# Optimization experiments

Hardware: AMD Instinct MI355X
Metric: run time of the kernel (lower is better)

Reference implementation:

```python
import jax, jax.numpy as jnp
import numpy as np


def _nearest_resize(x, Hl, Wl):
    # x: [B, Hf, Wf] -> [B, Hl, Wl], PyTorch F.interpolate(mode='nearest') semantics:
    # src_idx = floor(out_idx * in_size / out_size)
    B, Hf, Wf = x.shape
    ri = (jnp.arange(Hl) * Hf) // Hl
    ci = (jnp.arange(Wl) * Wf) // Wl
    return x[:, ri[:, None], ci[None, :]]


def _nearest_centroid(f, c):
    # f: [B, C, H, W], c: [K, C]
    # argmin_k ||f - c_k||_2 over channels == argmin of squared distance
    f2 = jnp.sum(f * f, axis=1)                       # [B, H, W]
    c2 = jnp.sum(c * c, axis=1)                       # [K]
    cross = jnp.einsum('bchw,kc->bkhw', f, c)         # [B, K, H, W]
    d2 = f2[:, None] - 2.0 * cross + c2[None, :, None, None]
    return jnp.argmin(d2, axis=1)                     # [B, H, W] int


def setup_inputs() -> dict:
    key = jax.random.key(0)
    k1, k2, k3, k4, k5, k6 = jax.random.split(key, 6)
    B, C, Hf, Wf = 4, 256, 64, 128
    K = 19  # class_num
    Hl, Wl = 512, 1024
    return {
        'feature_s2t': jax.random.normal(k1, (B, C, Hf, Wf), dtype=jnp.float32),
        'feature_target': jax.random.normal(k2, (B, C, Hf, Wf), dtype=jnp.float32),
        'label_s2t': jax.random.randint(k3, (B, Hl, Wl), 0, K, dtype=jnp.int64) if jax.config.jax_enable_x64 else jax.random.randint(k3, (B, Hl, Wl), 0, K, dtype=jnp.int32),
        'label_target': jax.random.randint(k4, (B, Hl, Wl), 0, K, dtype=jnp.int32),
        'centroid_s2t': jax.random.normal(k5, (K, C), dtype=jnp.float32),
        'centroid_target': jax.random.normal(k6, (K, C), dtype=jnp.float32),
    }


def reference(feature_s2t, feature_target, label_s2t, label_target, centroid_s2t, centroid_target):
    # feature_s2t is matched against the TARGET-domain centroids and vice versa
    # (cross assignment, exactly as in the torch forward).
    mask_s2t = _nearest_centroid(feature_s2t, centroid_target)     # [B, Hf, Wf]
    mask_target = _nearest_centroid(feature_target, centroid_s2t)  # [B, Hf, Wf]
    Hl, Wl = label_s2t.shape[1], label_s2t.shape[2]
    mask_s2t = _nearest_resize(mask_s2t, Hl, Wl).astype(jnp.int32)
    Hl2, Wl2 = label_target.shape[1], label_target.shape[2]
    mask_target = _nearest_resize(mask_target, Hl2, Wl2).astype(jnp.int32)
    return (mask_s2t, mask_target)
```

## Files before the change

### kernel.cpp

```cpp
#include <hip/hip_runtime.h>

#define K   19
#define C   256
#define HF  64
#define WF  128
#define HW  (HF * WF)
#define BB  4
#define HL  512
#define WL  1024

#define TAU 0.015f

__global__ __launch_bounds__(512, 4) void centroid_mask_kernel(
    const float* __restrict__ feat0,
    const float* __restrict__ feat1,
    const float* __restrict__ cent0,
    const float* __restrict__ cent1,
    int* __restrict__ out)
{
    __shared__ float  part[8 * K * 64];
    __shared__ double c2p[K][8];
    __shared__ double sc2d[K];
    __shared__ float  sc2f[K];

    const int map = blockIdx.y;
    const float* __restrict__ feat = (map == 0) ? feat0 : feat1;
    const float* __restrict__ cent = (map == 0) ? cent0 : cent1;

    const int tid  = threadIdx.x;
    const int lane = tid & 63;
    const int wv   = __builtin_amdgcn_readfirstlane(tid >> 6);

    if (tid < K * 8) {
        const int k = tid >> 3, sl = tid & 7;
        const float* cp = cent + k * C + sl * 32;
        double s = 0.0;
        #pragma unroll
        for (int j = 0; j < 32; ++j) { double v = (double)cp[j]; s = fma(v, v, s); }
        c2p[k][sl] = s;
    }

    const int p  = blockIdx.x * 64 + lane;
    const int hw = p & (HW - 1);
    const int b  = p >> 13;
    const int cbase = wv * 32;

    const float* __restrict__ fp = feat + (size_t)b * C * HW + (size_t)cbase * HW + hw;
    float f[32];
    #pragma unroll
    for (int i = 0; i < 32; ++i) f[i] = fp[(size_t)i * HW];
    #pragma unroll
    for (int i = 0; i < 32; ++i) asm volatile("" : "+v"(f[i]));

    float* __restrict__ pw = &part[(wv * K) * 64 + lane];
    #pragma unroll
    for (int k = 0; k < K; ++k) {
        const float* __restrict__ ck = cent + (size_t)k * C + cbase;
        float a0 = 0.f, a1 = 0.f, a2 = 0.f, a3 = 0.f;
        #pragma unroll
        for (int j = 0; j < 8; ++j) {
            a0 = fmaf(f[4*j+0], ck[4*j+0], a0);
            a1 = fmaf(f[4*j+1], ck[4*j+1], a1);
            a2 = fmaf(f[4*j+2], ck[4*j+2], a2);
            a3 = fmaf(f[4*j+3], ck[4*j+3], a3);
        }
        pw[k * 64] = (a0 + a1) + (a2 + a3);
    }
    __syncthreads();

    if (tid < K) {
        double s = 0.0;
        #pragma unroll
        for (int j = 0; j < 8; ++j) s += c2p[tid][j];
        sc2d[tid] = s;
        sc2f[tid] = (float)s;
    }
    __syncthreads();

    if (tid < 64) {
        const int pix = tid;
        float d[K];
        #pragma unroll
        for (int k = 0; k < K; ++k) {
            float s = 0.f;
            #pragma unroll
            for (int w8 = 0; w8 < 8; ++w8)
                s += part[(w8 * K + k) * 64 + pix];
            d[k] = sc2f[k] - 2.0f * s;
        }
        int best = 0; float m1 = d[0];
        #pragma unroll
        for (int k = 1; k < K; ++k) if (d[k] < m1) { m1 = d[k]; best = k; }

        unsigned cmask = 0u;
        #pragma unroll
        for (int k = 0; k < K; ++k) if (d[k] - m1 < TAU) cmask |= (1u << k);

        const bool need = (cmask & (cmask - 1)) != 0u;
        unsigned long long ball = __ballot(need);
        while (ball) {
            const int px = (int)__builtin_ctzll(ball);
            ball &= ball - 1;
            const unsigned pm  = __shfl(cmask, px, 64);
            const int      phw = __shfl(hw,    px, 64);
            const int      pb  = __shfl(b,     px, 64);
            const float* __restrict__ fcol = feat + (size_t)pb * C * HW + phw;

            const int c0 = tid << 2;
            double pf[4];
            #pragma unroll
            for (int j = 0; j < 4; ++j)
                pf[j] = (double)fcol[(size_t)(c0 + j) * HW];

            double bd = 1e300; int bi = 0;
            unsigned mm = pm;
            while (mm) {
                const int k = (int)__builtin_ctz(mm);
                mm &= mm - 1;
                const float* __restrict__ ck = cent + (size_t)k * C + c0;
                double s = 0.0;
                #pragma unroll
                for (int j = 0; j < 4; ++j)
                    s = fma(pf[j], (double)ck[j], s);
                #pragma unroll
                for (int off = 1; off < 64; off <<= 1)
                    s += __shfl_xor(s, off, 64);
                const double dk = sc2d[k] - 2.0 * s;
                if (dk < bd) { bd = dk; bi = k; }
            }
            if (tid == px) best = bi;
        }

        const int w = hw & (WF - 1);
        const int h = hw >> 7;
        int4 v = make_int4(best, best, best, best);
        int* __restrict__ ob = out + (size_t)map * (BB * HL * WL)
                                   + (size_t)b * (HL * WL)
                                   + (size_t)(h * 8) * WL + (size_t)(w * 8);
        #pragma unroll
        for (int r = 0; r < 8; ++r) {
            *(int4*)(ob + (size_t)r * WL)     = v;
            *(int4*)(ob + (size_t)r * WL + 4) = v;
        }
    }
}

extern "C" void kernel_launch(void* const* d_in, const int* in_sizes, int n_in,
                              void* d_out, int out_size, void* d_ws, size_t ws_size,
                              hipStream_t stream) {
    const float* feature_s2t     = (const float*)d_in[0];
    const float* feature_target  = (const float*)d_in[1];
    const float* centroid_s2t    = (const float*)d_in[4];
    const float* centroid_target = (const float*)d_in[5];
    int* out = (int*)d_out;

    dim3 grid(32768 / 64, 2);
    dim3 block(512);
    hipLaunchKernelGGL(centroid_mask_kernel, grid, block, 0, stream,
                       feature_s2t, feature_target,
                       centroid_target, centroid_s2t, out);
}
```

Before: 26.84 us.

## Spread argmin and writes across all waves, defer ambiguous pixels to resolve kernel

```diff
diff --git a/kernel.cpp b/kernel.cpp
--- a/kernel.cpp
+++ b/kernel.cpp
@@ -10,27 +10,194 @@
 #define WL  1024
 
 #define TAU 0.015f
+#define CAP 65536
+#define WS_NEED (4u + 4u * (CAP + 1))
 
 __global__ __launch_bounds__(512, 4) void centroid_mask_kernel(
     const float* __restrict__ feat0,
     const float* __restrict__ feat1,
     const float* __restrict__ cent0,
     const float* __restrict__ cent1,
+    int* __restrict__ out,
+    unsigned* __restrict__ wlist)
+{
+    __shared__ float  part[8 * K * 64];
+    __shared__ double c2p[K][8];
+    __shared__ float  sc2f[K];
+
+    const int map = blockIdx.y;
+    const float* __restrict__ feat = (map == 0) ? feat0 : feat1;
+    const float* __restrict__ cent = (map == 0) ? cent0 : cent1;
+
+    const int tid  = threadIdx.x;
+    const int lane = tid & 63;
+    const int wv   = __builtin_amdgcn_readfirstlane(tid >> 6);
+
+    if (tid < K * 8) {
+        const int k = tid >> 3, sl = tid & 7;
+        const float* cp = cent + k * C + sl * 32;
+        double s = 0.0;
+        #pragma unroll
+        for (int j = 0; j < 32; ++j) { double v = (double)cp[j]; s = fma(v, v, s); }
+        c2p[k][sl] = s;
+    }
+
+    const int p  = blockIdx.x * 64 + lane;
+    const int hw = p & (HW - 1);
+    const int b  = p >> 13;
+    const int cbase = wv * 32;
+
+    const float* __restrict__ fp = feat + (size_t)b * C * HW + (size_t)cbase * HW + hw;
+    float f[32];
+    #pragma unroll
+    for (int i = 0; i < 32; ++i) f[i] = fp[(size_t)i * HW];
+    #pragma unroll
+    for (int i = 0; i < 32; ++i) asm volatile("" : "+v"(f[i]));
+
+    float* __restrict__ pw = &part[(wv * K) * 64 + lane];
+    #pragma unroll
+    for (int k = 0; k < K; ++k) {
+        const float* __restrict__ ck = cent + (size_t)k * C + cbase;
+        float a0 = 0.f, a1 = 0.f, a2 = 0.f, a3 = 0.f;
+        #pragma unroll
+        for (int j = 0; j < 8; ++j) {
+            a0 = fmaf(f[4*j+0], ck[4*j+0], a0);
+            a1 = fmaf(f[4*j+1], ck[4*j+1], a1);
+            a2 = fmaf(f[4*j+2], ck[4*j+2], a2);
+            a3 = fmaf(f[4*j+3], ck[4*j+3], a3);
+        }
+        pw[k * 64] = (a0 + a1) + (a2 + a3);
+    }
+    __syncthreads();
+
+    if (tid < K) {
+        double s = 0.0;
+        #pragma unroll
+        for (int j = 0; j < 8; ++j) s += c2p[tid][j];
+        sc2f[tid] = (float)s;
+    }
+    __syncthreads();
+
+    {
+        const int pl = lane >> 3;
+        const int j  = lane & 7;
+        const int px = 8 * wv + pl;
+
+        float d0, d1, d2 = 1e30f;
+        {
+            float s = 0.f;
+            #pragma unroll
+            for (int w8 = 0; w8 < 8; ++w8) s += part[(w8 * K + j) * 64 + px];
+            d0 = sc2f[j] - 2.0f * s;
+        }
+        {
+            float s = 0.f;
+            #pragma unroll
+            for (int w8 = 0; w8 < 8; ++w8) s += part[(w8 * K + j + 8) * 64 + px];
+            d1 = sc2f[j + 8] - 2.0f * s;
+        }
+        if (j < 3) {
+            float s = 0.f;
+            #pragma unroll
+            for (int w8 = 0; w8 < 8; ++w8) s += part[(w8 * K + j + 16) * 64 + px];
+            d2 = sc2f[j + 16] - 2.0f * s;
+        }
+
+        float dm = d0; int km = j;
+        if (d1 < dm) { dm = d1; km = j + 8; }
+        if (j < 3 && d2 < dm) { dm = d2; km = j + 16; }
+
+        #pragma unroll
+        for (int off = 1; off < 8; off <<= 1) {
+            float od = __shfl_xor(dm, off, 64);
+            int   ok = __shfl_xor(km, off, 64);
+            if (od < dm || (od == dm && ok < km)) { dm = od; km = ok; }
+        }
+
+        int cnt = (int)(d0 - dm < TAU) + (int)(d1 - dm < TAU)
+                + (int)(j < 3 && (d2 - dm < TAU));
+        #pragma unroll
+        for (int off = 1; off < 8; off <<= 1) cnt += __shfl_xor(cnt, off, 64);
+
+        const int pp  = blockIdx.x * 64 + px;
+        const int phw = pp & (HW - 1);
+        const int pb  = pp >> 13;
+
+        if (cnt >= 2 && j == 0) {
+            unsigned idx = atomicAdd(wlist, 1u);
+            if (idx < CAP)
+                wlist[1 + idx] = ((unsigned)map << 15) | ((unsigned)pb << 13)
+                               | (unsigned)phw;
+        }
+
+        const int w = phw & (WF - 1);
+        const int h = phw >> 7;
+        int4 v = make_int4(km, km, km, km);
+        int* __restrict__ ob = out + (size_t)map * (BB * HL * WL)
+                                   + (size_t)pb * (HL * WL)
+                                   + (size_t)(h * 8 + j) * WL + (size_t)(w * 8);
+        *(int4*)(ob)     = v;
+        *(int4*)(ob + 4) = v;
+    }
+}
+
+__global__ __launch_bounds__(64) void resolve_kernel(
+    const float* __restrict__ feat0, const float* __restrict__ feat1,
+    const float* __restrict__ cent0, const float* __restrict__ cent1,
+    const unsigned* __restrict__ wlist,
+    int* __restrict__ out)
+{
+    unsigned cnt = wlist[0];
+    if (cnt > CAP) cnt = CAP;
+    const int l = threadIdx.x;
+
+    for (unsigned i = blockIdx.x; i < cnt; i += gridDim.x) {
+        const unsigned e = wlist[1 + i];
+        const int map = (e >> 15) & 1;
+        const int b   = (e >> 13) & 3;
+        const int hw  = e & (HW - 1);
+        const float* __restrict__ feat = map ? feat1 : feat0;
+        const float* __restrict__ cent = map ? cent1 : cent0;
+
+        const int c0 = l << 2;
+        double pf[4];
+        #pragma unroll
+        for (int q = 0; q < 4; ++q)
+            pf[q] = (double)feat[(size_t)b * C * HW + (size_t)(c0 + q) * HW + hw];
+
+        double bd = 1e300; int bi = 0;
+        for (int k = 0; k < K; ++k) {
+            const float4 cc = *(const float4*)(cent + (size_t)k * C + c0);
+            double s = 0.0, t;
+            t = pf[0] - (double)cc.x; s = fma(t, t, s);
+            t = pf[1] - (double)cc.y; s = fma(t, t, s);
+            t = pf[2] - (double)cc.z; s = fma(t, t, s);
+            t = pf[3] - (double)cc.w; s = fma(t, t, s);
+            #pragma unroll
+            for (int off = 1; off < 64; off <<= 1) s += __shfl_xor(s, off, 64);
+            if (s < bd) { bd = s; bi = k; }
+        }
+
+        const int w = hw & (WF - 1), h = hw >> 7;
+        out[(size_t)map * (BB * HL * WL) + (size_t)b * (HL * WL)
+            + (size_t)(h * 8 + (l >> 3)) * WL + (size_t)(w * 8) + (l & 7)] = bi;
+    }
+}
+
+__global__ __launch_bounds__(512, 4) void centroid_mask_kernel_nows(
+    const float* __restrict__ feat0, const float* __restrict__ feat1,
+    const float* __restrict__ cent0, const float* __restrict__ cent1,
     int* __restrict__ out)
 {
     __shared__ float  part[8 * K * 64];
     __shared__ double c2p[K][8];
     __shared__ double sc2d[K];
     __shared__ float  sc2f[K];
-
     const int map = blockIdx.y;
     const float* __restrict__ feat = (map == 0) ? feat0 : feat1;
     const float* __restrict__ cent = (map == 0) ? cent0 : cent1;
-
-    const int tid  = threadIdx.x;
-    const int lane = tid & 63;
-    const int wv   = __builtin_amdgcn_readfirstlane(tid >> 6);
-
+    const int tid = threadIdx.x, lane = tid & 63;
+    const int wv = __builtin_amdgcn_readfirstlane(tid >> 6);
     if (tid < K * 8) {
         const int k = tid >> 3, sl = tid & 7;
         const float* cp = cent + k * C + sl * 32;
@@ -39,19 +206,12 @@
         for (int j = 0; j < 32; ++j) { double v = (double)cp[j]; s = fma(v, v, s); }
         c2p[k][sl] = s;
     }
-
-    const int p  = blockIdx.x * 64 + lane;
-    const int hw = p & (HW - 1);
-    const int b  = p >> 13;
-    const int cbase = wv * 32;
-
+    const int p = blockIdx.x * 64 + lane;
+    const int hw = p & (HW - 1), b = p >> 13, cbase = wv * 32;
     const float* __restrict__ fp = feat + (size_t)b * C * HW + (size_t)cbase * HW + hw;
     float f[32];
     #pragma unroll
     for (int i = 0; i < 32; ++i) f[i] = fp[(size_t)i * HW];
-    #pragma unroll
-    for (int i = 0; i < 32; ++i) asm volatile("" : "+v"(f[i]));
-
     float* __restrict__ pw = &part[(wv * K) * 64 + lane];
     #pragma unroll
     for (int k = 0; k < K; ++k) {
@@ -67,16 +227,13 @@
         pw[k * 64] = (a0 + a1) + (a2 + a3);
     }
     __syncthreads();
-
     if (tid < K) {
         double s = 0.0;
         #pragma unroll
         for (int j = 0; j < 8; ++j) s += c2p[tid][j];
-        sc2d[tid] = s;
-        sc2f[tid] = (float)s;
+        sc2d[tid] = s; sc2f[tid] = (float)s;
     }
     __syncthreads();
-
     if (tid < 64) {
         const int pix = tid;
         float d[K];
@@ -84,18 +241,15 @@
         for (int k = 0; k < K; ++k) {
             float s = 0.f;
             #pragma unroll
-            for (int w8 = 0; w8 < 8; ++w8)
-                s += part[(w8 * K + k) * 64 + pix];
+            for (int w8 = 0; w8 < 8; ++w8) s += part[(w8 * K + k) * 64 + pix];
             d[k] = sc2f[k] - 2.0f * s;
         }
         int best = 0; float m1 = d[0];
         #pragma unroll
         for (int k = 1; k < K; ++k) if (d[k] < m1) { m1 = d[k]; best = k; }
-
         unsigned cmask = 0u;
         #pragma unroll
         for (int k = 0; k < K; ++k) if (d[k] - m1 < TAU) cmask |= (1u << k);
-
         const bool need = (cmask & (cmask - 1)) != 0u;
         unsigned long long ball = __ballot(need);
         while (ball) {
@@ -105,13 +259,10 @@
             const int      phw = __shfl(hw,    px, 64);
             const int      pb  = __shfl(b,     px, 64);
             const float* __restrict__ fcol = feat + (size_t)pb * C * HW + phw;
-
             const int c0 = tid << 2;
             double pf[4];
             #pragma unroll
-            for (int j = 0; j < 4; ++j)
-                pf[j] = (double)fcol[(size_t)(c0 + j) * HW];
-
+            for (int j = 0; j < 4; ++j) pf[j] = (double)fcol[(size_t)(c0 + j) * HW];
             double bd = 1e300; int bi = 0;
             unsigned mm = pm;
             while (mm) {
@@ -120,22 +271,17 @@
                 const float* __restrict__ ck = cent + (size_t)k * C + c0;
                 double s = 0.0;
                 #pragma unroll
-                for (int j = 0; j < 4; ++j)
-                    s = fma(pf[j], (double)ck[j], s);
+                for (int j = 0; j < 4; ++j) s = fma(pf[j], (double)ck[j], s);
                 #pragma unroll
-                for (int off = 1; off < 64; off <<= 1)
-                    s += __shfl_xor(s, off, 64);
+                for (int off = 1; off < 64; off <<= 1) s += __shfl_xor(s, off, 64);
                 const double dk = sc2d[k] - 2.0 * s;
                 if (dk < bd) { bd = dk; bi = k; }
             }
             if (tid == px) best = bi;
         }
-
-        const int w = hw & (WF - 1);
-        const int h = hw >> 7;
+        const int w = hw & (WF - 1), h = hw >> 7;
         int4 v = make_int4(best, best, best, best);
-        int* __restrict__ ob = out + (size_t)map * (BB * HL * WL)
-                                   + (size_t)b * (HL * WL)
+        int* __restrict__ ob = out + (size_t)map * (BB * HL * WL) + (size_t)b * (HL * WL)
                                    + (size_t)(h * 8) * WL + (size_t)(w * 8);
         #pragma unroll
         for (int r = 0; r < 8; ++r) {
@@ -154,9 +300,18 @@
     const float* centroid_target = (const float*)d_in[5];
     int* out = (int*)d_out;
 
-    dim3 grid(32768 / 64, 2);
-    dim3 block(512);
-    hipLaunchKernelGGL(centroid_mask_kernel, grid, block, 0, stream,
-                       feature_s2t, feature_target,
-                       centroid_target, centroid_s2t, out);
+    if (ws_size >= (size_t)WS_NEED) {
+        unsigned* wlist = (unsigned*)d_ws;
+        hipMemsetAsync(d_ws, 0, 4, stream);
+        hipLaunchKernelGGL(centroid_mask_kernel, dim3(512, 2), dim3(512), 0, stream,
+                           feature_s2t, feature_target,
+                           centroid_target, centroid_s2t, out, wlist);
+        hipLaunchKernelGGL(resolve_kernel, dim3(512), dim3(64), 0, stream,
+                           feature_s2t, feature_target,
+                           centroid_target, centroid_s2t, wlist, out);
+    } else {
+        hipLaunchKernelGGL(centroid_mask_kernel_nows, dim3(512, 2), dim3(512), 0, stream,
+                           feature_s2t, feature_target,
+                           centroid_target, centroid_s2t, out);
+    }
 }
```

Result: slower. 44.81 us (+67.0%).

## Spread argmin epilogue and output writes across all eight waves

Applied to the files above, without the earlier changes.

```diff
diff --git a/kernel.cpp b/kernel.cpp
--- a/kernel.cpp
+++ b/kernel.cpp
@@ -20,7 +20,6 @@
 {
     __shared__ float  part[8 * K * 64];
     __shared__ double c2p[K][8];
-    __shared__ double sc2d[K];
     __shared__ float  sc2f[K];
 
     const int map = blockIdx.y;
@@ -72,77 +71,98 @@
         double s = 0.0;
         #pragma unroll
         for (int j = 0; j < 8; ++j) s += c2p[tid][j];
-        sc2d[tid] = s;
         sc2f[tid] = (float)s;
     }
     __syncthreads();
 
-    if (tid < 64) {
-        const int pix = tid;
-        float d[K];
+    const int pl = lane >> 3;
+    const int j  = lane & 7;
+    const int px = 8 * wv + pl;
+
+    float d0, d1, d2 = 1e30f;
+    {
+        float s = 0.f;
         #pragma unroll
-        for (int k = 0; k < K; ++k) {
-            float s = 0.f;
+        for (int w8 = 0; w8 < 8; ++w8) s += part[(w8 * K + j) * 64 + px];
+        d0 = sc2f[j] - 2.0f * s;
+    }
+    {
+        float s = 0.f;
+        #pragma unroll
+        for (int w8 = 0; w8 < 8; ++w8) s += part[(w8 * K + j + 8) * 64 + px];
+        d1 = sc2f[j + 8] - 2.0f * s;
+    }
+    if (j < 3) {
+        float s = 0.f;
+        #pragma unroll
+        for (int w8 = 0; w8 < 8; ++w8) s += part[(w8 * K + j + 16) * 64 + px];
+        d2 = sc2f[j + 16] - 2.0f * s;
+    }
+
+    float dm = d0; int km = j;
+    if (d1 < dm) { dm = d1; km = j + 8; }
+    if (j < 3 && d2 < dm) { dm = d2; km = j + 16; }
+
+    #pragma unroll
+    for (int off = 1; off < 8; off <<= 1) {
+        float od = __shfl_xor(dm, off, 64);
+        int   ok = __shfl_xor(km, off, 64);
+        if (od < dm || (od == dm && ok < km)) { dm = od; km = ok; }
+    }
+
+    unsigned cm = ((unsigned)(d0 - dm < TAU) << j)
+                | ((unsigned)(d1 - dm < TAU) << (j + 8))
+                | ((j < 3 && (d2 - dm < TAU)) ? (1u << (j + 16)) : 0u);
+    #pragma unroll
+    for (int off = 1; off < 8; off <<= 1) cm |= __shfl_xor(cm, off, 64);
+
+    const bool need = (cm & (cm - 1u)) != 0u;
+    unsigned long long ball = __ballot(need && (j == 0));
+    while (ball) {
+        const int src = (int)__builtin_ctzll(ball);
+        ball &= ball - 1;
+        const unsigned pm  = __shfl(cm, src, 64);
+        const int      fpl = src >> 3;
+        const int      fpp = blockIdx.x * 64 + 8 * wv + fpl;
+        const int      fhw = fpp & (HW - 1);
+        const int      fb  = fpp >> 13;
+        const float* __restrict__ fcol = feat + (size_t)fb * C * HW + fhw;
+
+        const int c0 = lane << 2;
+        double pf[4];
+        #pragma unroll
+        for (int q = 0; q < 4; ++q)
+            pf[q] = (double)fcol[(size_t)(c0 + q) * HW];
+
+        double bd = 1e300; int bi = 0;
+        unsigned mm = pm;
+        while (mm) {
+            const int k = (int)__builtin_ctz(mm);
+            mm &= mm - 1;
+            const float4 cc = *(const float4*)(cent + (size_t)k * C + c0);
+            double s = 0.0, t;
+            t = pf[0] - (double)cc.x; s = fma(t, t, s);
+            t = pf[1] - (double)cc.y; s = fma(t, t, s);
+            t = pf[2] - (double)cc.z; s = fma(t, t, s);
+            t = pf[3] - (double)cc.w; s = fma(t, t, s);
             #pragma unroll
-            for (int w8 = 0; w8 < 8; ++w8)
-                s += part[(w8 * K + k) * 64 + pix];
-            d[k] = sc2f[k] - 2.0f * s;
+            for (int off = 1; off < 64; off <<= 1) s += __shfl_xor(s, off, 64);
+            if (s < bd) { bd = s; bi = k; }
         }
-        int best = 0; float m1 = d[0];
-        #pragma unroll
-        for (int k = 1; k < K; ++k) if (d[k] < m1) { m1 = d[k]; best = k; }
+        if (pl == fpl) km = bi;
+    }
 
-        unsigned cmask = 0u;
-        #pragma unroll
-        for (int k = 0; k < K; ++k) if (d[k] - m1 < TAU) cmask |= (1u << k);
-
-        const bool need = (cmask & (cmask - 1)) != 0u;
-        unsigned long long ball = __ballot(need);
-        while (ball) {
-            const int px = (int)__builtin_ctzll(ball);
-            ball &= ball - 1;
-            const unsigned pm  = __shfl(cmask, px, 64);
-            const int      phw = __shfl(hw,    px, 64);
-            const int      pb  = __shfl(b,     px, 64);
-            const float* __restrict__ fcol = feat + (size_t)pb * C * HW + phw;
-
-            const int c0 = tid << 2;
-            double pf[4];
-            #pragma unroll
-            for (int j = 0; j < 4; ++j)
-                pf[j] = (double)fcol[(size_t)(c0 + j) * HW];
-
-            double bd = 1e300; int bi = 0;
-            unsigned mm = pm;
-            while (mm) {
-                const int k = (int)__builtin_ctz(mm);
-                mm &= mm - 1;
-                const float* __restrict__ ck = cent + (size_t)k * C + c0;
-                double s = 0.0;
-                #pragma unroll
-                for (int j = 0; j < 4; ++j)
-                    s = fma(pf[j], (double)ck[j], s);
-                #pragma unroll
-                for (int off = 1; off < 64; off <<= 1)
-                    s += __shfl_xor(s, off, 64);
-                const double dk = sc2d[k] - 2.0 * s;
-                if (dk < bd) { bd = dk; bi = k; }
-            }
-            if (tid == px) best = bi;
-        }
-
-        const int w = hw & (WF - 1);
-        const int h = hw >> 7;
-        int4 v = make_int4(best, best, best, best);
-        int* __restrict__ ob = out + (size_t)map * (BB * HL * WL)
-                                   + (size_t)b * (HL * WL)
-                                   + (size_t)(h * 8) * WL + (size_t)(w * 8);
-        #pragma unroll
-        for (int r = 0; r < 8; ++r) {
-            *(int4*)(ob + (size_t)r * WL)     = v;
-            *(int4*)(ob + (size_t)r * WL + 4) = v;
-        }
-    }
+    const int pp  = blockIdx.x * 64 + px;
+    const int phw = pp & (HW - 1);
+    const int pb  = pp >> 13;
+    const int w = phw & (WF - 1);
+    const int h = phw >> 7;
+    int4 v = make_int4(km, km, km, km);
+    int* __restrict__ ob = out + (size_t)map * (BB * HL * WL)
+                               + (size_t)pb * (HL * WL)
+                               + (size_t)(h * 8 + j) * WL + (size_t)(w * 8);
+    *(int4*)(ob)     = v;
+    *(int4*)(ob + 4) = v;
 }
 
 extern "C" void kernel_launch(void* const* d_in, const int* in_sizes, int n_in,
```

Result: slower. 31.42 us (+17.1%).

## Halve block to 4 waves with 64 channels each, streaming features in chunks

Applied to the files above, without the earlier changes.

```diff
diff --git a/kernel.cpp b/kernel.cpp
--- a/kernel.cpp
+++ b/kernel.cpp
@@ -11,14 +11,14 @@
 
 #define TAU 0.015f
 
-__global__ __launch_bounds__(512, 4) void centroid_mask_kernel(
+__global__ __launch_bounds__(256, 4) void centroid_mask_kernel(
     const float* __restrict__ feat0,
     const float* __restrict__ feat1,
     const float* __restrict__ cent0,
     const float* __restrict__ cent1,
     int* __restrict__ out)
 {
-    __shared__ float  part[8 * K * 64];
+    __shared__ float  part[4 * K * 64];
     __shared__ double c2p[K][8];
     __shared__ double sc2d[K];
     __shared__ float  sc2f[K];
@@ -43,29 +43,36 @@
     const int p  = blockIdx.x * 64 + lane;
     const int hw = p & (HW - 1);
     const int b  = p >> 13;
-    const int cbase = wv * 32;
+    const int cb = wv * 64;
 
-    const float* __restrict__ fp = feat + (size_t)b * C * HW + (size_t)cbase * HW + hw;
-    float f[32];
+    const float* __restrict__ fp = feat + (size_t)b * C * HW + (size_t)cb * HW + hw;
+    const float* __restrict__ cw = cent + cb;
+
+    float acc[K];
     #pragma unroll
-    for (int i = 0; i < 32; ++i) f[i] = fp[(size_t)i * HW];
+    for (int k = 0; k < K; ++k) acc[k] = 0.f;
+
     #pragma unroll
-    for (int i = 0; i < 32; ++i) asm volatile("" : "+v"(f[i]));
+    for (int ch = 0; ch < 8; ++ch) {
+        float f8[8];
+        #pragma unroll
+        for (int i = 0; i < 8; ++i)
+            f8[i] = fp[(size_t)(ch * 8 + i) * HW];
+        #pragma unroll
+        for (int k = 0; k < K; ++k) {
+            const float* __restrict__ ck = cw + (size_t)k * C + ch * 8;
+            float a = acc[k];
+            a = fmaf(f8[0], ck[0], a); a = fmaf(f8[1], ck[1], a);
+            a = fmaf(f8[2], ck[2], a); a = fmaf(f8[3], ck[3], a);
+            a = fmaf(f8[4], ck[4], a); a = fmaf(f8[5], ck[5], a);
+            a = fmaf(f8[6], ck[6], a); a = fmaf(f8[7], ck[7], a);
+            acc[k] = a;
+        }
+    }
 
     float* __restrict__ pw = &part[(wv * K) * 64 + lane];
     #pragma unroll
-    for (int k = 0; k < K; ++k) {
-        const float* __restrict__ ck = cent + (size_t)k * C + cbase;
-        float a0 = 0.f, a1 = 0.f, a2 = 0.f, a3 = 0.f;
-        #pragma unroll
-        for (int j = 0; j < 8; ++j) {
-            a0 = fmaf(f[4*j+0], ck[4*j+0], a0);
-            a1 = fmaf(f[4*j+1], ck[4*j+1], a1);
-            a2 = fmaf(f[4*j+2], ck[4*j+2], a2);
-            a3 = fmaf(f[4*j+3], ck[4*j+3], a3);
-        }
-        pw[k * 64] = (a0 + a1) + (a2 + a3);
-    }
+    for (int k = 0; k < K; ++k) pw[k * 64] = acc[k];
     __syncthreads();
 
     if (tid < K) {
@@ -82,10 +89,8 @@
         float d[K];
         #pragma unroll
         for (int k = 0; k < K; ++k) {
-            float s = 0.f;
-            #pragma unroll
-            for (int w8 = 0; w8 < 8; ++w8)
-                s += part[(w8 * K + k) * 64 + pix];
+            const float s = (part[(0 * K + k) * 64 + pix] + part[(1 * K + k) * 64 + pix])
+                          + (part[(2 * K + k) * 64 + pix] + part[(3 * K + k) * 64 + pix]);
             d[k] = sc2f[k] - 2.0f * s;
         }
         int best = 0; float m1 = d[0];
@@ -155,7 +160,7 @@
     int* out = (int*)d_out;
 
     dim3 grid(32768 / 64, 2);
-    dim3 block(512);
+    dim3 block(256);
     hipLaunchKernelGGL(centroid_mask_kernel, grid, block, 0, stream,
                        feature_s2t, feature_target,
                        centroid_target, centroid_s2t, out);
```

Result: faster. 25.38 us (-5.4%).
